# Performance work log

Measured on AMD Instinct MI355X. Metric: run time of the kernel, lower is better.

The kernel has to match this reference:

```python
import jax, jax.numpy as jnp
import numpy as np
import math

D = 512; H = 8; NL = 6; VOCAB = 256; NC = 10; L = 1024; B = 4
DK = D // H
SCALE = math.sqrt(DK)
EMB_SCALE = math.sqrt(D)
EPS = 1e-5


def _pos_encoding(seq_len, d_model):
    pos = jnp.arange(seq_len, dtype=jnp.float32)[:, None]
    div = jnp.exp(-jnp.arange(0, d_model, 2, dtype=jnp.float32) / d_model * math.log(10000.0))
    pe = jnp.zeros((seq_len, d_model), dtype=jnp.float32)
    pe = pe.at[:, 0::2].set(jnp.sin(pos * div))
    pe = pe.at[:, 1::2].set(jnp.cos(pos * div))
    return pe


def _layer_norm(x, g, b):
    m = jnp.mean(x, axis=-1, keepdims=True)
    v = jnp.mean(jnp.square(x - m), axis=-1, keepdims=True)
    return (x - m) * jax.lax.rsqrt(v + EPS) * g + b


def setup_inputs() -> dict:
    key = jax.random.key(0)
    ks = jax.random.split(key, 18)
    s = 0.02  # keep activations in a sane range so softmax is not saturated
    return {
        "tokens": jax.random.randint(ks[0], (B, L), 0, VOCAB, dtype=jnp.int32),
        "emb_table": jax.random.normal(ks[1], (VOCAB, D), jnp.float32) * s,
        "Wq": jax.random.normal(ks[2], (NL, D, D), jnp.float32) * s,
        "bq": jax.random.normal(ks[3], (NL, D), jnp.float32) * s,
        "Wkv": jax.random.normal(ks[4], (NL, 2 * D, D), jnp.float32) * s,
        "bkv": jax.random.normal(ks[5], (NL, 2 * D), jnp.float32) * s,
        "Wo": jax.random.normal(ks[6], (NL, D, D), jnp.float32) * s,
        "bo": jax.random.normal(ks[7], (NL, D), jnp.float32) * s,
        "ln1_g": jnp.ones((NL, D), jnp.float32),
        "ln1_b": jnp.zeros((NL, D), jnp.float32),
        "W1": jax.random.normal(ks[8], (NL, 4 * D, D), jnp.float32) * s,
        "b1": jax.random.normal(ks[9], (NL, 4 * D), jnp.float32) * s,
        "W2": jax.random.normal(ks[10], (NL, D, 4 * D), jnp.float32) * s,
        "b2": jax.random.normal(ks[11], (NL, D), jnp.float32) * s,
        "ln2_g": jnp.ones((NL, D), jnp.float32),
        "ln2_b": jnp.zeros((NL, D), jnp.float32),
        "Wc": jax.random.normal(ks[12], (NC, D), jnp.float32) * s,
        "bc": jax.random.normal(ks[13], (NC,), jnp.float32) * s,
    }


def reference(tokens, emb_table, Wq, bq, Wkv, bkv, Wo, bo, ln1_g, ln1_b,
              W1, b1, W2, b2, ln2_g, ln2_b, Wc, bc):
    seq_len = tokens.shape[1]
    pe = _pos_encoding(seq_len, D)  # [L, D]
    x = emb_table[tokens] * EMB_SCALE + pe[None]  # [B, L, D]  (dropout = identity in eval)

    def block(x, p):
        wq, bq_, wkv, bkv_, wo, bo_, g1, be1, w1, bb1, w2, bb2, g2, be2 = p
        h = _layer_norm(x, g1, be1)
        q = h @ wq.T + bq_                       # [B, L, D]
        kv = h @ wkv.T + bkv_                    # [B, L, 2D]
        k, v = kv[..., :D], kv[..., D:]
        # split heads: [B, H, L, dk]
        q = q.reshape(*q.shape[:2], H, DK).transpose(0, 2, 1, 3)
        k = k.reshape(*k.shape[:2], H, DK).transpose(0, 2, 1, 3)
        v = v.reshape(*v.shape[:2], H, DK).transpose(0, 2, 1, 3)
        score = jnp.einsum('bhqd,bhkd->bhqk', q, k) / SCALE  # [B, H, L, L]
        attn = jax.nn.softmax(score, axis=-1)
        av = jnp.einsum('bhqk,bhkd->bhqd', attn, v)
        av = av.transpose(0, 2, 1, 3).reshape(*x.shape)      # merge heads
        x = x + (av @ wo.T + bo_)
        h2 = _layer_norm(x, g2, be2)
        ffn = jax.nn.relu(h2 @ w1.T + bb1) @ w2.T + bb2
        x = x + ffn
        return x, None

    params = (Wq, bq, Wkv, bkv, Wo, bo, ln1_g, ln1_b, W1, b1, W2, b2, ln2_g, ln2_b)
    x, _ = jax.lax.scan(block, x, params)
    return x @ Wc.T + bc  # [B, L, NC]
```

## Files before the change

### kernel.cpp

```cpp
#include <hip/hip_runtime.h>
#include <math.h>

#define D 512
#define HEADS 8
#define NLAYER 6
#define LSEQ 1024
#define BATCH 4
#define DKH 64
#define MTOK (BATCH*LSEQ)
#define EPS 1e-5f
#define EMB_SCALE 22.627416997969522f
#define INV_SCALE 0.125f

typedef __attribute__((ext_vector_type(8))) __bf16 bf16x8;
typedef __attribute__((ext_vector_type(4))) float f32x4;

__device__ __forceinline__ unsigned short f2bf(float x) {
    union { float f; unsigned u; } v; v.f = x;
    unsigned r = (v.u + 0x7FFFu + ((v.u >> 16) & 1u)) >> 16;
    return (unsigned short)r;
}
__device__ __forceinline__ unsigned pack2(float a, float b) {
    return (unsigned)f2bf(a) | ((unsigned)f2bf(b) << 16);
}
__device__ __forceinline__ void gl_lds16(const unsigned short* g, unsigned short* l) {
    __builtin_amdgcn_global_load_lds(
        (const __attribute__((address_space(1))) unsigned*)g,
        (__attribute__((address_space(3))) unsigned*)l, 16, 0, 0);
}
__device__ __forceinline__ void gload16(bf16x8& d, const unsigned short* p) {
    asm volatile("global_load_dwordx4 %0, %1, off" : "=v"(d) : "v"(p));
}

__global__ __launch_bounds__(128) void embed_kernel(
    const int* __restrict__ tokens, const float* __restrict__ emb,
    float* __restrict__ x)
{
    int row = blockIdx.x;
    int pos = row & (LSEQ - 1);
    int tok = tokens[row];
    int c = threadIdx.x * 4;
    float4 e = *(const float4*)(emb + (size_t)tok * D + c);
    float o[4] = {e.x, e.y, e.z, e.w};
#pragma unroll
    for (int i = 0; i < 4; ++i) {
        int col = c + i;
        int ii = col & ~1;
        float dv = expf(-(float)ii * (9.210340371976184f / (float)D));
        float a = (float)pos * dv;
        float pe = (col & 1) ? cosf(a) : sinf(a);
        o[i] = o[i] * EMB_SCALE + pe;
    }
    float4 r; r.x = o[0]; r.y = o[1]; r.z = o[2]; r.w = o[3];
    *(float4*)(x + (size_t)row * D + c) = r;
}

__global__ __launch_bounds__(256) void ln_kernel(
    const float* __restrict__ x, const float* __restrict__ g,
    const float* __restrict__ b, unsigned short* __restrict__ h)
{
    int lane = threadIdx.x & 63;
    int row = blockIdx.x * 4 + (threadIdx.x >> 6);
    const float* xr = x + (size_t)row * D + lane * 8;
    float4 v0 = *(const float4*)(xr);
    float4 v1 = *(const float4*)(xr + 4);
    float s = v0.x + v0.y + v0.z + v0.w + v1.x + v1.y + v1.z + v1.w;
#pragma unroll
    for (int off = 32; off; off >>= 1) s += __shfl_xor(s, off, 64);
    float m = s * (1.0f / D);
    float d0 = v0.x - m, d1 = v0.y - m, d2 = v0.z - m, d3 = v0.w - m;
    float d4 = v1.x - m, d5 = v1.y - m, d6 = v1.z - m, d7 = v1.w - m;
    float ss = d0*d0 + d1*d1 + d2*d2 + d3*d3 + d4*d4 + d5*d5 + d6*d6 + d7*d7;
#pragma unroll
    for (int off = 32; off; off >>= 1) ss += __shfl_xor(ss, off, 64);
    float inv = rsqrtf(ss * (1.0f / D) + EPS);
    const float* gp = g + lane * 8;
    const float* bp = b + lane * 8;
    float4 g0 = *(const float4*)(gp), g1 = *(const float4*)(gp + 4);
    float4 b0 = *(const float4*)(bp), b1 = *(const float4*)(bp + 4);
    uint4 o;
    o.x = pack2(d0 * inv * g0.x + b0.x, d1 * inv * g0.y + b0.y);
    o.y = pack2(d2 * inv * g0.z + b0.z, d3 * inv * g0.w + b0.w);
    o.z = pack2(d4 * inv * g1.x + b1.x, d5 * inv * g1.y + b1.y);
    o.w = pack2(d6 * inv * g1.z + b1.z, d7 * inv * g1.w + b1.w);
    *(uint4*)(h + (size_t)row * D + lane * 8) = o;
}

__global__ __launch_bounds__(256) void wconv_kernel(
    const float* __restrict__ Wq, const float* __restrict__ Wkv,
    const float* __restrict__ Wo, const float* __restrict__ W1,
    const float* __restrict__ W2, const float* __restrict__ bq,
    const float* __restrict__ bkv, unsigned short* __restrict__ dst,
    float* __restrict__ bias_out)
{
    if (blockIdx.x == 1536) {
        for (int i = threadIdx.x; i < 1536; i += 256)
            bias_out[i] = (i < 512) ? bq[i] : bkv[i - 512];
        return;
    }
    int gid = blockIdx.x * 256 + threadIdx.x;
    int e = gid * 8;
    const float* src;
    if      (e < 262144)  src = Wq  + e;
    else if (e < 786432)  src = Wkv + (e - 262144);
    else if (e < 1048576) src = Wo  + (e - 786432);
    else if (e < 2097152) src = W1  + (e - 1048576);
    else                  src = W2  + (e - 2097152);
    float4 a = *(const float4*)src;
    float4 b = *(const float4*)(src + 4);
    uint4 o;
    o.x = pack2(a.x, a.y); o.y = pack2(a.z, a.w);
    o.z = pack2(b.x, b.y); o.w = pack2(b.z, b.w);
    *(uint4*)(dst + e) = o;
}

template<int OMODE, int BM>
__global__ __launch_bounds__(256) void gemm_bf16(
    const unsigned short* __restrict__ A, const unsigned short* __restrict__ W,
    const float* __restrict__ bias, const float* __restrict__ X,
    void* __restrict__ C, void* __restrict__ C2, void* __restrict__ C3,
    int M, int N, int K)
{
    constexpr int WM = BM / 64;
    constexpr int WN = 4 / WM;
    constexpr int NI = 8 / WN;
    __shared__ __align__(16) unsigned short As[2][BM * 64];
    __shared__ __align__(16) unsigned short Bs[2][128 * 64];
    const int tid = threadIdx.x;
    const int wave = tid >> 6, lane = tid & 63;
    const int quad = lane >> 4, l16 = lane & 15;
    const int wm = wave / WN, wn = wave % WN;
    const int bm = blockIdx.y * BM, bn = blockIdx.x * 128;

    const int rS  = tid >> 3;
    const int csw = (((tid & 7) ^ (rS & 7)) << 3);
    const unsigned short* Asrc = A + (size_t)(bm + rS) * K + csw;
    const unsigned short* Bsrc = W + (size_t)(bn + rS) * K + csw;

    f32x4 acc[4][NI];
#pragma unroll
    for (int mi = 0; mi < 4; ++mi)
#pragma unroll
        for (int ni = 0; ni < NI; ++ni) acc[mi][ni] = (f32x4){0.f, 0.f, 0.f, 0.f};

    const int nt = K >> 6;

#pragma unroll
    for (int i = 0; i < BM / 32; ++i)
        gl_lds16(Asrc + (size_t)(i * 32) * K, &As[0][i * 2048 + tid * 8]);
#pragma unroll
    for (int i = 0; i < 4; ++i)
        gl_lds16(Bsrc + (size_t)(i * 32) * K, &Bs[0][i * 2048 + tid * 8]);
    __syncthreads();

    for (int t = 0; t < nt; ++t) {
        const int cur = t & 1;
        if (t + 1 < nt) {
            const int k0 = (t + 1) << 6;
#pragma unroll
            for (int i = 0; i < BM / 32; ++i)
                gl_lds16(Asrc + (size_t)(i * 32) * K + k0, &As[cur ^ 1][i * 2048 + tid * 8]);
#pragma unroll
            for (int i = 0; i < 4; ++i)
                gl_lds16(Bsrc + (size_t)(i * 32) * K + k0, &Bs[cur ^ 1][i * 2048 + tid * 8]);
        }
#pragma unroll
        for (int kc = 0; kc < 2; ++kc) {
            const int gch = (kc << 2) | quad;
            bf16x8 af[4], bfr[NI];
#pragma unroll
            for (int mi = 0; mi < 4; ++mi) {
                const int ra = wm * 64 + mi * 16 + l16;
                af[mi] = *(const bf16x8*)&As[cur][ra * 64 + ((gch ^ (ra & 7)) << 3)];
            }
#pragma unroll
            for (int ni = 0; ni < NI; ++ni) {
                const int rb = wn * (128 / WN) + ni * 16 + l16;
                bfr[ni] = *(const bf16x8*)&Bs[cur][rb * 64 + ((gch ^ (rb & 7)) << 3)];
            }
#pragma unroll
            for (int mi = 0; mi < 4; ++mi)
#pragma unroll
                for (int ni = 0; ni < NI; ++ni)
                    acc[mi][ni] = __builtin_amdgcn_mfma_f32_16x16x32_bf16(
                        af[mi], bfr[ni], acc[mi][ni], 0, 0, 0);
        }
        __syncthreads();
    }

    const int er = bm + wm * 64;
    const int ec = bn + wn * (128 / WN);

    if (OMODE == 0) {
        float* Cf = (float*)C;
#pragma unroll
        for (int ni = 0; ni < NI; ++ni) {
            int c = ec + ni * 16 + l16;
            float bv = bias[c];
#pragma unroll
            for (int mi = 0; mi < 4; ++mi)
#pragma unroll
                for (int r = 0; r < 4; ++r) {
                    int m = er + mi * 16 + quad * 4 + r;
                    Cf[(size_t)m * N + c] = acc[mi][ni][r] + bv + X[(size_t)m * N + c];
                }
        }
    } else if (OMODE == 1) {
        unsigned short* Cb = (unsigned short*)C;
#pragma unroll
        for (int ni = 0; ni < NI; ++ni) {
            int c = ec + ni * 16 + l16;
            float bv = bias[c];
#pragma unroll
            for (int mi = 0; mi < 4; ++mi)
#pragma unroll
                for (int r = 0; r < 4; ++r) {
                    int m = er + mi * 16 + quad * 4 + r;
                    Cb[(size_t)m * N + c] = f2bf(fmaxf(acc[mi][ni][r] + bv, 0.f));
                }
        }
    } else {
        if (bn < 512) {
            unsigned short* Qp = (unsigned short*)C;
#pragma unroll
            for (int ni = 0; ni < NI; ++ni) {
                int c = ec + ni * 16 + l16;
                float bv = bias[c];
                int hh = c >> 6, dd = c & 63;
                size_t cbase = (size_t)(dd >> 5) * 512 + (size_t)((dd >> 3) & 3) * 128 + (dd & 7);
#pragma unroll
                for (int mi = 0; mi < 4; ++mi)
#pragma unroll
                    for (int r = 0; r < 4; ++r) {
                        int m = er + mi * 16 + quad * 4 + r;
                        int b = m >> 10, t = m & 1023;
                        Qp[(size_t)(b * 8 + hh) * 65536 + (size_t)(t >> 4) * 1024
                           + cbase + (size_t)(t & 15) * 8] =
                            f2bf((acc[mi][ni][r] + bv) * INV_SCALE);
                    }
            }
        } else if (bn < 1024) {
            unsigned short* Kp = (unsigned short*)C2;
#pragma unroll
            for (int ni = 0; ni < NI; ++ni) {
                int c = ec + ni * 16 + l16;
                float bv = bias[c];
                int c2 = c - 512;
                int hh = c2 >> 6, dd = c2 & 63;
                size_t cbase = (size_t)(dd >> 5) * 512 + (size_t)((dd >> 3) & 3) * 128 + (dd & 7);
#pragma unroll
                for (int mi = 0; mi < 4; ++mi)
#pragma unroll
                    for (int r = 0; r < 4; ++r) {
                        int m = er + mi * 16 + quad * 4 + r;
                        int b = m >> 10, t = m & 1023;
                        Kp[(size_t)(b * 8 + hh) * 65536 + (size_t)(t >> 4) * 1024
                           + cbase + (size_t)(t & 15) * 8] =
                            f2bf(acc[mi][ni][r] + bv);
                    }
            }
        } else {
            unsigned short* Vp = (unsigned short*)C3;
#pragma unroll
            for (int ni = 0; ni < NI; ++ni) {
                int c = ec + ni * 16 + l16;
                float bv = bias[c];
                int c2 = c - 1024;
                int hh = c2 >> 6, dd = c2 & 63;
                size_t dbase = (size_t)(dd >> 4) * 16384 + (size_t)(dd & 15) * 8;
#pragma unroll
                for (int mi = 0; mi < 4; ++mi) {
                    int t0 = er + mi * 16 + quad * 4;
                    int b = t0 >> 10, tt = t0 & 1023;
                    ushort4 o;
                    o.x = f2bf(acc[mi][ni][0] + bv);
                    o.y = f2bf(acc[mi][ni][1] + bv);
                    o.z = f2bf(acc[mi][ni][2] + bv);
                    o.w = f2bf(acc[mi][ni][3] + bv);
                    *(ushort4*)(Vp + (size_t)(b * 8 + hh) * 65536 + dbase
                                + (size_t)(tt >> 5) * 512
                                + (size_t)((tt >> 3) & 3) * 128 + (tt & 7)) = o;
                }
            }
        }
    }
}

__global__ __launch_bounds__(256, 1) void attn_mfma(
    const unsigned short* __restrict__ Qb, const unsigned short* __restrict__ Kb,
    const unsigned short* __restrict__ Vt, unsigned short* __restrict__ av)
{
    __shared__ float Ol[4][16][68];
    __shared__ float Ls[4][16];
    const int tid = threadIdx.x;
    const int wave = tid >> 6, lane = tid & 63;
    const int quad = lane >> 4, l16 = lane & 15;
    const int bh = blockIdx.x & 31;
    const int b = bh >> 3, h = bh & 7;
    const int q0 = (blockIdx.x >> 5) * 16;

    const unsigned short* qp = Qb + (size_t)bh * 65536 + (size_t)q0 * 64 + lane * 8;
    const unsigned short* kbase = Kb + (size_t)bh * 65536 + lane * 8;
    const unsigned short* vbase = Vt + (size_t)bh * 65536 + lane * 8;

    const int sA  = ((((2 * quad) & 3) << 4) + l16) << 2;
    const int sB2 = ((((2 * quad + 1) & 3) << 4) + l16) << 2;

    f32x4 o[4];
#pragma unroll
    for (int nf = 0; nf < 4; ++nf) o[nf] = (f32x4){0.f, 0.f, 0.f, 0.f};
    float lp = 0.f;

    const int j0 = wave * 256;

    bf16x8 qf0, qf1;
    gload16(qf0, qp);
    gload16(qf1, qp + 512);

    bf16x8 kc[2][8], vf[2][8];
#pragma unroll
    for (int nf = 0; nf < 4; ++nf) {
        gload16(kc[0][2 * nf],     kbase + (size_t)j0 * 64 + nf * 1024);
        gload16(kc[0][2 * nf + 1], kbase + (size_t)j0 * 64 + nf * 1024 + 512);
        gload16(vf[0][2 * nf],     vbase + (size_t)j0 * 16 + nf * 16384);
        gload16(vf[0][2 * nf + 1], vbase + (size_t)j0 * 16 + nf * 16384 + 512);
    }

#pragma unroll
    for (int it = 0; it < 4; ++it) {
        const int cur = it & 1, nxt = cur ^ 1;
        if (it < 3) {
            const int jn = j0 + (it + 1) * 64;
#pragma unroll
            for (int nf = 0; nf < 4; ++nf) {
                gload16(kc[nxt][2 * nf],     kbase + (size_t)jn * 64 + nf * 1024);
                gload16(kc[nxt][2 * nf + 1], kbase + (size_t)jn * 64 + nf * 1024 + 512);
                gload16(vf[nxt][2 * nf],     vbase + (size_t)jn * 16 + nf * 16384);
                gload16(vf[nxt][2 * nf + 1], vbase + (size_t)jn * 16 + nf * 16384 + 512);
            }
        }
        if (it < 3) asm volatile("s_waitcnt vmcnt(16)" ::: "memory");
        else        asm volatile("s_waitcnt vmcnt(0)"  ::: "memory");
        __builtin_amdgcn_sched_barrier(0);
        f32x4 s[4];
#pragma unroll
        for (int nf = 0; nf < 4; ++nf) {
            f32x4 z = {0.f, 0.f, 0.f, 0.f};
            z = __builtin_amdgcn_mfma_f32_16x16x32_bf16(kc[cur][2 * nf], qf0, z, 0, 0, 0);
            z = __builtin_amdgcn_mfma_f32_16x16x32_bf16(kc[cur][2 * nf + 1], qf1, z, 0, 0, 0);
            s[nf] = z;
        }
        unsigned pk01[4], pk23[4];
#pragma unroll
        for (int nf = 0; nf < 4; ++nf) {
            float p0 = __expf(s[nf][0]);
            float p1 = __expf(s[nf][1]);
            float p2 = __expf(s[nf][2]);
            float p3 = __expf(s[nf][3]);
            lp += (p0 + p1) + (p2 + p3);
            pk01[nf] = pack2(p0, p1);
            pk23[nf] = pack2(p2, p3);
        }
        union PU { unsigned d[4]; bf16x8 v; } f0, f1;
        {
            unsigned a0, a1;
            a0 = (unsigned)__builtin_amdgcn_ds_bpermute(sA,  (int)pk01[0]);
            a1 = (unsigned)__builtin_amdgcn_ds_bpermute(sA,  (int)pk01[1]);
            f0.d[0] = (quad < 2) ? a0 : a1;
            a0 = (unsigned)__builtin_amdgcn_ds_bpermute(sA,  (int)pk23[0]);
            a1 = (unsigned)__builtin_amdgcn_ds_bpermute(sA,  (int)pk23[1]);
            f0.d[1] = (quad < 2) ? a0 : a1;
            a0 = (unsigned)__builtin_amdgcn_ds_bpermute(sB2, (int)pk01[0]);
            a1 = (unsigned)__builtin_amdgcn_ds_bpermute(sB2, (int)pk01[1]);
            f0.d[2] = (quad < 2) ? a0 : a1;
            a0 = (unsigned)__builtin_amdgcn_ds_bpermute(sB2, (int)pk23[0]);
            a1 = (unsigned)__builtin_amdgcn_ds_bpermute(sB2, (int)pk23[1]);
            f0.d[3] = (quad < 2) ? a0 : a1;
            a0 = (unsigned)__builtin_amdgcn_ds_bpermute(sA,  (int)pk01[2]);
            a1 = (unsigned)__builtin_amdgcn_ds_bpermute(sA,  (int)pk01[3]);
            f1.d[0] = (quad < 2) ? a0 : a1;
            a0 = (unsigned)__builtin_amdgcn_ds_bpermute(sA,  (int)pk23[2]);
            a1 = (unsigned)__builtin_amdgcn_ds_bpermute(sA,  (int)pk23[3]);
            f1.d[1] = (quad < 2) ? a0 : a1;
            a0 = (unsigned)__builtin_amdgcn_ds_bpermute(sB2, (int)pk01[2]);
            a1 = (unsigned)__builtin_amdgcn_ds_bpermute(sB2, (int)pk01[3]);
            f1.d[2] = (quad < 2) ? a0 : a1;
            a0 = (unsigned)__builtin_amdgcn_ds_bpermute(sB2, (int)pk23[2]);
            a1 = (unsigned)__builtin_amdgcn_ds_bpermute(sB2, (int)pk23[3]);
            f1.d[3] = (quad < 2) ? a0 : a1;
        }
#pragma unroll
        for (int nf = 0; nf < 4; ++nf) {
            o[nf] = __builtin_amdgcn_mfma_f32_16x16x32_bf16(f0.v, vf[cur][2 * nf], o[nf], 0, 0, 0);
            o[nf] = __builtin_amdgcn_mfma_f32_16x16x32_bf16(f1.v, vf[cur][2 * nf + 1], o[nf], 0, 0, 0);
        }
    }
#pragma unroll
    for (int nf = 0; nf < 4; ++nf)
#pragma unroll
        for (int r = 0; r < 4; ++r)
            Ol[wave][quad * 4 + r][nf * 16 + l16] = o[nf][r];
    float ts = lp;
    ts += __shfl_xor(ts, 16, 64);
    ts += __shfl_xor(ts, 32, 64);
    if (quad == 0) Ls[wave][l16] = ts;
    __syncthreads();
    float denom[4];
#pragma unroll
    for (int r = 0; r < 4; ++r)
        denom[r] = Ls[0][quad * 4 + r] + Ls[1][quad * 4 + r]
                 + Ls[2][quad * 4 + r] + Ls[3][quad * 4 + r];
#pragma unroll
    for (int r = 0; r < 4; ++r) {
        int qq = quad * 4 + r;
        float v = Ol[0][qq][wave * 16 + l16] + Ol[1][qq][wave * 16 + l16]
                + Ol[2][qq][wave * 16 + l16] + Ol[3][qq][wave * 16 + l16];
        int q = q0 + qq;
        av[((size_t)(b * 1024 + q)) * D + h * 64 + wave * 16 + l16] =
            f2bf(v / denom[r]);
    }
}

__global__ __launch_bounds__(256) void cls_kernel(
    const float* __restrict__ x, const float* __restrict__ Wc,
    const float* __restrict__ bc, float* __restrict__ out)
{
    int lane = threadIdx.x & 63;
    int row = blockIdx.x * 4 + (threadIdx.x >> 6);
    const float* xr = x + (size_t)row * D + lane * 8;
    float4 v0 = *(const float4*)xr;
    float4 v1 = *(const float4*)(xr + 4);
    float acc[10];
#pragma unroll
    for (int c = 0; c < 10; ++c) {
        const float* wr = Wc + c * D + lane * 8;
        float4 w0 = *(const float4*)wr;
        float4 w1 = *(const float4*)(wr + 4);
        acc[c] = v0.x*w0.x + v0.y*w0.y + v0.z*w0.z + v0.w*w0.w
               + v1.x*w1.x + v1.y*w1.y + v1.z*w1.z + v1.w*w1.w;
    }
#pragma unroll
    for (int c = 0; c < 10; ++c)
#pragma unroll
        for (int off = 32; off; off >>= 1) acc[c] += __shfl_xor(acc[c], off, 64);
    if (lane == 0) {
#pragma unroll
        for (int c = 0; c < 10; ++c) out[(size_t)row * 10 + c] = acc[c] + bc[c];
    }
}

extern "C" void kernel_launch(void* const* d_in, const int* in_sizes, int n_in,
                              void* d_out, int out_size, void* d_ws, size_t ws_size,
                              hipStream_t stream)
{
    const int*   tokens = (const int*)  d_in[0];
    const float* emb    = (const float*)d_in[1];
    const float* Wq     = (const float*)d_in[2];
    const float* bq     = (const float*)d_in[3];
    const float* Wkv    = (const float*)d_in[4];
    const float* bkv    = (const float*)d_in[5];
    const float* Wo     = (const float*)d_in[6];
    const float* bo     = (const float*)d_in[7];
    const float* ln1g   = (const float*)d_in[8];
    const float* ln1b   = (const float*)d_in[9];
    const float* W1     = (const float*)d_in[10];
    const float* b1     = (const float*)d_in[11];
    const float* W2     = (const float*)d_in[12];
    const float* b2     = (const float*)d_in[13];
    const float* ln2g   = (const float*)d_in[14];
    const float* ln2b   = (const float*)d_in[15];
    const float* Wc     = (const float*)d_in[16];
    const float* bc     = (const float*)d_in[17];
    float* out = (float*)d_out;

    float* x  = (float*)d_ws;
    unsigned short* hb  = (unsigned short*)(x + (size_t)MTOK * D);
    unsigned short* Qb  = hb  + (size_t)MTOK * D;
    unsigned short* Kb  = Qb  + (size_t)32 * 1024 * 64;
    unsigned short* Vt  = Kb  + (size_t)32 * 1024 * 64;
    unsigned short* avb = Vt  + (size_t)32 * 1024 * 64;
    unsigned short* f1b = Qb;
    unsigned short* wl  = avb + (size_t)32 * 1024 * 64;
    float* wbias = (float*)(wl + (size_t)3145728);

    const size_t oWo = 786432, oW1 = 1048576, oW2 = 2097152;

    embed_kernel<<<MTOK, 128, 0, stream>>>(tokens, emb, x);

    for (int l = 0; l < NLAYER; ++l) {
        wconv_kernel<<<1537, 256, 0, stream>>>(
            Wq  + (size_t)l * 262144,  Wkv + (size_t)l * 524288,
            Wo  + (size_t)l * 262144,  W1  + (size_t)l * 1048576,
            W2  + (size_t)l * 1048576, bq + (size_t)l * 512,
            bkv + (size_t)l * 1024, wl, wbias);
        ln_kernel<<<MTOK / 4, 256, 0, stream>>>(x, ln1g + l * D, ln1b + l * D, hb);
        gemm_bf16<2,128><<<dim3(12, 32), 256, 0, stream>>>(
            hb, wl, wbias, nullptr, Qb, Kb, Vt, MTOK, 1536, 512);
        attn_mfma<<<2048, 256, 0, stream>>>(Qb, Kb, Vt, avb);
        gemm_bf16<0,64><<<dim3(4, 64), 256, 0, stream>>>(
            avb, wl + oWo, bo + l * D, x, x, nullptr, nullptr, MTOK, D, D);
        ln_kernel<<<MTOK / 4, 256, 0, stream>>>(x, ln2g + l * D, ln2b + l * D, hb);
        gemm_bf16<1,128><<<dim3(16, 32), 256, 0, stream>>>(
            hb, wl + oW1, b1 + l * 4 * D, nullptr, f1b, nullptr, nullptr, MTOK, 4 * D, D);
        gemm_bf16<0,64><<<dim3(4, 64), 256, 0, stream>>>(
            f1b, wl + oW2, b2 + l * D, x, x, nullptr, nullptr, MTOK, D, 4 * D);
    }

    cls_kernel<<<MTOK / 4, 256, 0, stream>>>(x, Wc, bc, out);
}
```

Before: 842.2 us.

## Process two 16-query tiles per attention block to reuse K/V register loads

Each attention block now handles 32 queries instead of 16, so every K and V fragment loaded into registers feeds two sets of score and output MFMAs. The grid is halved to 1024 blocks and the LDS reduction buffers are doubled. This cuts global K/V traffic per query in half. The cost is more registers and fewer blocks to fill the GPU, which may lower occupancy.

```diff
diff --git a/kernel.cpp b/kernel.cpp
--- a/kernel.cpp
+++ b/kernel.cpp
@@ -290,32 +290,36 @@
     const unsigned short* __restrict__ Qb, const unsigned short* __restrict__ Kb,
     const unsigned short* __restrict__ Vt, unsigned short* __restrict__ av)
 {
-    __shared__ float Ol[4][16][68];
-    __shared__ float Ls[4][16];
+    __shared__ float Ol[4][32][68];
+    __shared__ float Ls[4][32];
     const int tid = threadIdx.x;
     const int wave = tid >> 6, lane = tid & 63;
     const int quad = lane >> 4, l16 = lane & 15;
     const int bh = blockIdx.x & 31;
     const int b = bh >> 3, h = bh & 7;
-    const int q0 = (blockIdx.x >> 5) * 16;
-
-    const unsigned short* qp = Qb + (size_t)bh * 65536 + (size_t)q0 * 64 + lane * 8;
+    const int q0 = (blockIdx.x >> 5) * 32;
+
+    const unsigned short* qp = Qb + (size_t)bh * 65536 + (size_t)(q0 >> 4) * 1024 + lane * 8;
     const unsigned short* kbase = Kb + (size_t)bh * 65536 + lane * 8;
     const unsigned short* vbase = Vt + (size_t)bh * 65536 + lane * 8;
 
     const int sA  = ((((2 * quad) & 3) << 4) + l16) << 2;
     const int sB2 = ((((2 * quad + 1) & 3) << 4) + l16) << 2;
 
-    f32x4 o[4];
-#pragma unroll
-    for (int nf = 0; nf < 4; ++nf) o[nf] = (f32x4){0.f, 0.f, 0.f, 0.f};
-    float lp = 0.f;
+    f32x4 o[2][4];
+#pragma unroll
+    for (int qs = 0; qs < 2; ++qs)
+#pragma unroll
+        for (int nf = 0; nf < 4; ++nf) o[qs][nf] = (f32x4){0.f, 0.f, 0.f, 0.f};
+    float lp[2] = {0.f, 0.f};
 
     const int j0 = wave * 256;
 
-    bf16x8 qf0, qf1;
-    gload16(qf0, qp);
-    gload16(qf1, qp + 512);
+    bf16x8 qf[2][2];
+    gload16(qf[0][0], qp);
+    gload16(qf[0][1], qp + 512);
+    gload16(qf[1][0], qp + 1024);
+    gload16(qf[1][1], qp + 1536);
 
     bf16x8 kc[2][8], vf[2][8];
 #pragma unroll
@@ -342,83 +346,84 @@
         if (it < 3) asm volatile("s_waitcnt vmcnt(16)" ::: "memory");
         else        asm volatile("s_waitcnt vmcnt(0)"  ::: "memory");
         __builtin_amdgcn_sched_barrier(0);
-        f32x4 s[4];
-#pragma unroll
-        for (int nf = 0; nf < 4; ++nf) {
-            f32x4 z = {0.f, 0.f, 0.f, 0.f};
-            z = __builtin_amdgcn_mfma_f32_16x16x32_bf16(kc[cur][2 * nf], qf0, z, 0, 0, 0);
-            z = __builtin_amdgcn_mfma_f32_16x16x32_bf16(kc[cur][2 * nf + 1], qf1, z, 0, 0, 0);
-            s[nf] = z;
-        }
-        unsigned pk01[4], pk23[4];
-#pragma unroll
-        for (int nf = 0; nf < 4; ++nf) {
-            float p0 = __expf(s[nf][0]);
-            float p1 = __expf(s[nf][1]);
-            float p2 = __expf(s[nf][2]);
-            float p3 = __expf(s[nf][3]);
-            lp += (p0 + p1) + (p2 + p3);
-            pk01[nf] = pack2(p0, p1);
-            pk23[nf] = pack2(p2, p3);
-        }
-        union PU { unsigned d[4]; bf16x8 v; } f0, f1;
-        {
+        unsigned pk01[2][4], pk23[2][4];
+#pragma unroll
+        for (int nf = 0; nf < 4; ++nf)
+#pragma unroll
+            for (int qs = 0; qs < 2; ++qs) {
+                f32x4 z = {0.f, 0.f, 0.f, 0.f};
+                z = __builtin_amdgcn_mfma_f32_16x16x32_bf16(kc[cur][2 * nf], qf[qs][0], z, 0, 0, 0);
+                z = __builtin_amdgcn_mfma_f32_16x16x32_bf16(kc[cur][2 * nf + 1], qf[qs][1], z, 0, 0, 0);
+                float p0 = __expf(z[0]);
+                float p1 = __expf(z[1]);
+                float p2 = __expf(z[2]);
+                float p3 = __expf(z[3]);
+                lp[qs] += (p0 + p1) + (p2 + p3);
+                pk01[qs][nf] = pack2(p0, p1);
+                pk23[qs][nf] = pack2(p2, p3);
+            }
+#pragma unroll
+        for (int qs = 0; qs < 2; ++qs) {
+            union PU { unsigned d[4]; bf16x8 v; } f0, f1;
             unsigned a0, a1;
-            a0 = (unsigned)__builtin_amdgcn_ds_bpermute(sA,  (int)pk01[0]);
-            a1 = (unsigned)__builtin_amdgcn_ds_bpermute(sA,  (int)pk01[1]);
+            a0 = (unsigned)__builtin_amdgcn_ds_bpermute(sA,  (int)pk01[qs][0]);
+            a1 = (unsigned)__builtin_amdgcn_ds_bpermute(sA,  (int)pk01[qs][1]);
             f0.d[0] = (quad < 2) ? a0 : a1;
-            a0 = (unsigned)__builtin_amdgcn_ds_bpermute(sA,  (int)pk23[0]);
-            a1 = (unsigned)__builtin_amdgcn_ds_bpermute(sA,  (int)pk23[1]);
+            a0 = (unsigned)__builtin_amdgcn_ds_bpermute(sA,  (int)pk23[qs][0]);
+            a1 = (unsigned)__builtin_amdgcn_ds_bpermute(sA,  (int)pk23[qs][1]);
             f0.d[1] = (quad < 2) ? a0 : a1;
-            a0 = (unsigned)__builtin_amdgcn_ds_bpermute(sB2, (int)pk01[0]);
-            a1 = (unsigned)__builtin_amdgcn_ds_bpermute(sB2, (int)pk01[1]);
+            a0 = (unsigned)__builtin_amdgcn_ds_bpermute(sB2, (int)pk01[qs][0]);
+            a1 = (unsigned)__builtin_amdgcn_ds_bpermute(sB2, (int)pk01[qs][1]);
             f0.d[2] = (quad < 2) ? a0 : a1;
-            a0 = (unsigned)__builtin_amdgcn_ds_bpermute(sB2, (int)pk23[0]);
-            a1 = (unsigned)__builtin_amdgcn_ds_bpermute(sB2, (int)pk23[1]);
+            a0 = (unsigned)__builtin_amdgcn_ds_bpermute(sB2, (int)pk23[qs][0]);
+            a1 = (unsigned)__builtin_amdgcn_ds_bpermute(sB2, (int)pk23[qs][1]);
             f0.d[3] = (quad < 2) ? a0 : a1;
-            a0 = (unsigned)__builtin_amdgcn_ds_bpermute(sA,  (int)pk01[2]);
-            a1 = (unsigned)__builtin_amdgcn_ds_bpermute(sA,  (int)pk01[3]);
+            a0 = (unsigned)__builtin_amdgcn_ds_bpermute(sA,  (int)pk01[qs][2]);
+            a1 = (unsigned)__builtin_amdgcn_ds_bpermute(sA,  (int)pk01[qs][3]);
             f1.d[0] = (quad < 2) ? a0 : a1;
-            a0 = (unsigned)__builtin_amdgcn_ds_bpermute(sA,  (int)pk23[2]);
-            a1 = (unsigned)__builtin_amdgcn_ds_bpermute(sA,  (int)pk23[3]);
+            a0 = (unsigned)__builtin_amdgcn_ds_bpermute(sA,  (int)pk23[qs][2]);
+            a1 = (unsigned)__builtin_amdgcn_ds_bpermute(sA,  (int)pk23[qs][3]);
             f1.d[1] = (quad < 2) ? a0 : a1;
-            a0 = (unsigned)__builtin_amdgcn_ds_bpermute(sB2, (int)pk01[2]);
-            a1 = (unsigned)__builtin_amdgcn_ds_bpermute(sB2, (int)pk01[3]);
+            a0 = (unsigned)__builtin_amdgcn_ds_bpermute(sB2, (int)pk01[qs][2]);
+            a1 = (unsigned)__builtin_amdgcn_ds_bpermute(sB2, (int)pk01[qs][3]);
             f1.d[2] = (quad < 2) ? a0 : a1;
-            a0 = (unsigned)__builtin_amdgcn_ds_bpermute(sB2, (int)pk23[2]);
-            a1 = (unsigned)__builtin_amdgcn_ds_bpermute(sB2, (int)pk23[3]);
+            a0 = (unsigned)__builtin_amdgcn_ds_bpermute(sB2, (int)pk23[qs][2]);
+            a1 = (unsigned)__builtin_amdgcn_ds_bpermute(sB2, (int)pk23[qs][3]);
             f1.d[3] = (quad < 2) ? a0 : a1;
-        }
-#pragma unroll
-        for (int nf = 0; nf < 4; ++nf) {
-            o[nf] = __builtin_amdgcn_mfma_f32_16x16x32_bf16(f0.v, vf[cur][2 * nf], o[nf], 0, 0, 0);
-            o[nf] = __builtin_amdgcn_mfma_f32_16x16x32_bf16(f1.v, vf[cur][2 * nf + 1], o[nf], 0, 0, 0);
-        }
-    }
-#pragma unroll
-    for (int nf = 0; nf < 4; ++nf)
-#pragma unroll
-        for (int r = 0; r < 4; ++r)
-            Ol[wave][quad * 4 + r][nf * 16 + l16] = o[nf][r];
-    float ts = lp;
-    ts += __shfl_xor(ts, 16, 64);
-    ts += __shfl_xor(ts, 32, 64);
-    if (quad == 0) Ls[wave][l16] = ts;
+#pragma unroll
+            for (int nf = 0; nf < 4; ++nf) {
+                o[qs][nf] = __builtin_amdgcn_mfma_f32_16x16x32_bf16(f0.v, vf[cur][2 * nf], o[qs][nf], 0, 0, 0);
+                o[qs][nf] = __builtin_amdgcn_mfma_f32_16x16x32_bf16(f1.v, vf[cur][2 * nf + 1], o[qs][nf], 0, 0, 0);
+            }
+        }
+    }
+#pragma unroll
+    for (int qs = 0; qs < 2; ++qs)
+#pragma unroll
+        for (int nf = 0; nf < 4; ++nf)
+#pragma unroll
+            for (int r = 0; r < 4; ++r)
+                Ol[wave][qs * 16 + quad * 4 + r][nf * 16 + l16] = o[qs][nf][r];
+#pragma unroll
+    for (int qs = 0; qs < 2; ++qs) {
+        float ts = lp[qs];
+        ts += __shfl_xor(ts, 16, 64);
+        ts += __shfl_xor(ts, 32, 64);
+        if (quad == 0) Ls[wave][qs * 16 + l16] = ts;
+    }
     __syncthreads();
-    float denom[4];
-#pragma unroll
-    for (int r = 0; r < 4; ++r)
-        denom[r] = Ls[0][quad * 4 + r] + Ls[1][quad * 4 + r]
-                 + Ls[2][quad * 4 + r] + Ls[3][quad * 4 + r];
-#pragma unroll
-    for (int r = 0; r < 4; ++r) {
-        int qq = quad * 4 + r;
-        float v = Ol[0][qq][wave * 16 + l16] + Ol[1][qq][wave * 16 + l16]
-                + Ol[2][qq][wave * 16 + l16] + Ol[3][qq][wave * 16 + l16];
-        int q = q0 + qq;
-        av[((size_t)(b * 1024 + q)) * D + h * 64 + wave * 16 + l16] =
-            f2bf(v / denom[r]);
-    }
+#pragma unroll
+    for (int half = 0; half < 2; ++half)
+#pragma unroll
+        for (int r = 0; r < 4; ++r) {
+            int qq = half * 16 + quad * 4 + r;
+            float denom = Ls[0][qq] + Ls[1][qq] + Ls[2][qq] + Ls[3][qq];
+            float v = Ol[0][qq][wave * 16 + l16] + Ol[1][qq][wave * 16 + l16]
+                    + Ol[2][qq][wave * 16 + l16] + Ol[3][qq][wave * 16 + l16];
+            int q = q0 + qq;
+            av[((size_t)(b * 1024 + q)) * D + h * 64 + wave * 16 + l16] =
+                f2bf(v / denom);
+        }
 }
 
 __global__ __launch_bounds__(256) void cls_kernel(
@@ -496,7 +501,7 @@
         ln_kernel<<<MTOK / 4, 256, 0, stream>>>(x, ln1g + l * D, ln1b + l * D, hb);
         gemm_bf16<2,128><<<dim3(12, 32), 256, 0, stream>>>(
             hb, wl, wbias, nullptr, Qb, Kb, Vt, MTOK, 1536, 512);
-        attn_mfma<<<2048, 256, 0, stream>>>(Qb, Kb, Vt, avb);
+        attn_mfma<<<1024, 256, 0, stream>>>(Qb, Kb, Vt, avb);
         gemm_bf16<0,64><<<dim3(4, 64), 256, 0, stream>>>(
             avb, wl + oWo, bo + l * D, x, x, nullptr, nullptr, MTOK, D, D);
         ln_kernel<<<MTOK / 4, 256, 0, stream>>>(x, ln2g + l * D, ln2b + l * D, hb);
```

After: 810.8 us. -3.7%, faster.

## Share K/V tiles across waves via LDS in attention, each wave owning queries

Applied to the files above, without the earlier changes.

Restructures the attention kernel so each block handles 64 queries (16 per wave) and walks the full key sequence. K and V tiles are staged once per block into double-buffered LDS with global_load_lds and shared by all four waves. Previously each wave loaded its own quarter of the keys straight from global memory and the partial outputs were combined through LDS. This cuts global K/V traffic by 4x and removes the cross-wave reduction, at the cost of a barrier every iteration and a 4x smaller grid.

```diff
diff --git a/kernel.cpp b/kernel.cpp
--- a/kernel.cpp
+++ b/kernel.cpp
@@ -27,9 +27,6 @@
     __builtin_amdgcn_global_load_lds(
         (const __attribute__((address_space(1))) unsigned*)g,
         (__attribute__((address_space(3))) unsigned*)l, 16, 0, 0);
-}
-__device__ __forceinline__ void gload16(bf16x8& d, const unsigned short* p) {
-    asm volatile("global_load_dwordx4 %0, %1, off" : "=v"(d) : "v"(p));
 }
 
 __global__ __launch_bounds__(128) void embed_kernel(
@@ -286,77 +283,63 @@
     }
 }
 
-__global__ __launch_bounds__(256, 1) void attn_mfma(
+__global__ __launch_bounds__(256, 2) void attn_mfma(
     const unsigned short* __restrict__ Qb, const unsigned short* __restrict__ Kb,
     const unsigned short* __restrict__ Vt, unsigned short* __restrict__ av)
 {
-    __shared__ float Ol[4][16][68];
-    __shared__ float Ls[4][16];
+    __shared__ __align__(16) unsigned short Ks[2][4096];
+    __shared__ __align__(16) unsigned short Vs[2][4096];
     const int tid = threadIdx.x;
     const int wave = tid >> 6, lane = tid & 63;
     const int quad = lane >> 4, l16 = lane & 15;
     const int bh = blockIdx.x & 31;
     const int b = bh >> 3, h = bh & 7;
-    const int q0 = (blockIdx.x >> 5) * 16;
-
-    const unsigned short* qp = Qb + (size_t)bh * 65536 + (size_t)q0 * 64 + lane * 8;
-    const unsigned short* kbase = Kb + (size_t)bh * 65536 + lane * 8;
-    const unsigned short* vbase = Vt + (size_t)bh * 65536 + lane * 8;
+    const int q0 = (blockIdx.x >> 5) * 64 + wave * 16;
+
+    const unsigned short* qp   = Qb + (size_t)bh * 65536 + (size_t)(q0 >> 4) * 1024 + lane * 8;
+    const unsigned short* ksrc = Kb + (size_t)bh * 65536;
+    const unsigned short* vsrc = Vt + (size_t)bh * 65536;
 
     const int sA  = ((((2 * quad) & 3) << 4) + l16) << 2;
     const int sB2 = ((((2 * quad + 1) & 3) << 4) + l16) << 2;
 
+    bf16x8 qf0 = *(const bf16x8*)qp;
+    bf16x8 qf1 = *(const bf16x8*)(qp + 512);
+
     f32x4 o[4];
 #pragma unroll
     for (int nf = 0; nf < 4; ++nf) o[nf] = (f32x4){0.f, 0.f, 0.f, 0.f};
     float lp = 0.f;
 
-    const int j0 = wave * 256;
-
-    bf16x8 qf0, qf1;
-    gload16(qf0, qp);
-    gload16(qf1, qp + 512);
-
-    bf16x8 kc[2][8], vf[2][8];
-#pragma unroll
-    for (int nf = 0; nf < 4; ++nf) {
-        gload16(kc[0][2 * nf],     kbase + (size_t)j0 * 64 + nf * 1024);
-        gload16(kc[0][2 * nf + 1], kbase + (size_t)j0 * 64 + nf * 1024 + 512);
-        gload16(vf[0][2 * nf],     vbase + (size_t)j0 * 16 + nf * 16384);
-        gload16(vf[0][2 * nf + 1], vbase + (size_t)j0 * 16 + nf * 16384 + 512);
-    }
-
-#pragma unroll
-    for (int it = 0; it < 4; ++it) {
-        const int cur = it & 1, nxt = cur ^ 1;
-        if (it < 3) {
-            const int jn = j0 + (it + 1) * 64;
-#pragma unroll
-            for (int nf = 0; nf < 4; ++nf) {
-                gload16(kc[nxt][2 * nf],     kbase + (size_t)jn * 64 + nf * 1024);
-                gload16(kc[nxt][2 * nf + 1], kbase + (size_t)jn * 64 + nf * 1024 + 512);
-                gload16(vf[nxt][2 * nf],     vbase + (size_t)jn * 16 + nf * 16384);
-                gload16(vf[nxt][2 * nf + 1], vbase + (size_t)jn * 16 + nf * 16384 + 512);
-            }
-        }
-        if (it < 3) asm volatile("s_waitcnt vmcnt(16)" ::: "memory");
-        else        asm volatile("s_waitcnt vmcnt(0)"  ::: "memory");
-        __builtin_amdgcn_sched_barrier(0);
-        f32x4 s[4];
+    auto STAGE = [&](int j, int buf) {
+        gl_lds16(ksrc + (size_t)j * 64 + tid * 8,        &Ks[buf][tid * 8]);
+        gl_lds16(ksrc + (size_t)j * 64 + 2048 + tid * 8, &Ks[buf][2048 + tid * 8]);
+        gl_lds16(vsrc + (size_t)j * 16 + (size_t)(wave >> 1) * 16384
+                      + (wave & 1) * 512 + lane * 8,
+                 &Vs[buf][wave * 512 + lane * 8]);
+        gl_lds16(vsrc + (size_t)j * 16 + (size_t)((wave + 4) >> 1) * 16384
+                      + ((wave + 4) & 1) * 512 + lane * 8,
+                 &Vs[buf][2048 + wave * 512 + lane * 8]);
+    };
+
+    STAGE(0, 0);
+    __syncthreads();
+
+    for (int it = 0; it < 16; ++it) {
+        const int cur = it & 1;
+        if (it + 1 < 16) STAGE((it + 1) * 64, cur ^ 1);
+        unsigned pk01[4], pk23[4];
 #pragma unroll
         for (int nf = 0; nf < 4; ++nf) {
+            bf16x8 kc0 = *(const bf16x8*)&Ks[cur][nf * 1024 + lane * 8];
+            bf16x8 kc1 = *(const bf16x8*)&Ks[cur][nf * 1024 + 512 + lane * 8];
             f32x4 z = {0.f, 0.f, 0.f, 0.f};
-            z = __builtin_amdgcn_mfma_f32_16x16x32_bf16(kc[cur][2 * nf], qf0, z, 0, 0, 0);
-            z = __builtin_amdgcn_mfma_f32_16x16x32_bf16(kc[cur][2 * nf + 1], qf1, z, 0, 0, 0);
-            s[nf] = z;
-        }
-        unsigned pk01[4], pk23[4];
-#pragma unroll
-        for (int nf = 0; nf < 4; ++nf) {
-            float p0 = __expf(s[nf][0]);
-            float p1 = __expf(s[nf][1]);
-            float p2 = __expf(s[nf][2]);
-            float p3 = __expf(s[nf][3]);
+            z = __builtin_amdgcn_mfma_f32_16x16x32_bf16(kc0, qf0, z, 0, 0, 0);
+            z = __builtin_amdgcn_mfma_f32_16x16x32_bf16(kc1, qf1, z, 0, 0, 0);
+            float p0 = __expf(z[0]);
+            float p1 = __expf(z[1]);
+            float p2 = __expf(z[2]);
+            float p3 = __expf(z[3]);
             lp += (p0 + p1) + (p2 + p3);
             pk01[nf] = pack2(p0, p1);
             pk23[nf] = pack2(p2, p3);
@@ -391,33 +374,28 @@
         }
 #pragma unroll
         for (int nf = 0; nf < 4; ++nf) {
-            o[nf] = __builtin_amdgcn_mfma_f32_16x16x32_bf16(f0.v, vf[cur][2 * nf], o[nf], 0, 0, 0);
-            o[nf] = __builtin_amdgcn_mfma_f32_16x16x32_bf16(f1.v, vf[cur][2 * nf + 1], o[nf], 0, 0, 0);
-        }
-    }
-#pragma unroll
-    for (int nf = 0; nf < 4; ++nf)
-#pragma unroll
-        for (int r = 0; r < 4; ++r)
-            Ol[wave][quad * 4 + r][nf * 16 + l16] = o[nf][r];
+            bf16x8 vf0 = *(const bf16x8*)&Vs[cur][nf * 1024 + lane * 8];
+            bf16x8 vf1 = *(const bf16x8*)&Vs[cur][nf * 1024 + 512 + lane * 8];
+            o[nf] = __builtin_amdgcn_mfma_f32_16x16x32_bf16(f0.v, vf0, o[nf], 0, 0, 0);
+            o[nf] = __builtin_amdgcn_mfma_f32_16x16x32_bf16(f1.v, vf1, o[nf], 0, 0, 0);
+        }
+        __syncthreads();
+    }
+
     float ts = lp;
     ts += __shfl_xor(ts, 16, 64);
     ts += __shfl_xor(ts, 32, 64);
-    if (quad == 0) Ls[wave][l16] = ts;
-    __syncthreads();
-    float denom[4];
-#pragma unroll
-    for (int r = 0; r < 4; ++r)
-        denom[r] = Ls[0][quad * 4 + r] + Ls[1][quad * 4 + r]
-                 + Ls[2][quad * 4 + r] + Ls[3][quad * 4 + r];
+    union { float f; int i; } tsb; tsb.f = ts;
 #pragma unroll
     for (int r = 0; r < 4; ++r) {
-        int qq = quad * 4 + r;
-        float v = Ol[0][qq][wave * 16 + l16] + Ol[1][qq][wave * 16 + l16]
-                + Ol[2][qq][wave * 16 + l16] + Ol[3][qq][wave * 16 + l16];
-        int q = q0 + qq;
-        av[((size_t)(b * 1024 + q)) * D + h * 64 + wave * 16 + l16] =
-            f2bf(v / denom[r]);
+        union { int i; float f; } dv;
+        dv.i = __builtin_amdgcn_ds_bpermute((quad * 20 + r) << 2, tsb.i);
+        float inv = 1.0f / dv.f;
+        int q = q0 + quad * 4 + r;
+#pragma unroll
+        for (int nf = 0; nf < 4; ++nf)
+            av[((size_t)(b * 1024 + q)) * D + h * 64 + nf * 16 + l16] =
+                f2bf(o[nf][r] * inv);
     }
 }
 
@@ -496,7 +474,7 @@
         ln_kernel<<<MTOK / 4, 256, 0, stream>>>(x, ln1g + l * D, ln1b + l * D, hb);
         gemm_bf16<2,128><<<dim3(12, 32), 256, 0, stream>>>(
             hb, wl, wbias, nullptr, Qb, Kb, Vt, MTOK, 1536, 512);
-        attn_mfma<<<2048, 256, 0, stream>>>(Qb, Kb, Vt, avb);
+        attn_mfma<<<512, 256, 0, stream>>>(Qb, Kb, Vt, avb);
         gemm_bf16<0,64><<<dim3(4, 64), 256, 0, stream>>>(
             avb, wl + oWo, bo + l * D, x, x, nullptr, nullptr, MTOK, D, D);
         ln_kernel<<<MTOK / 4, 256, 0, stream>>>(x, ln2g + l * D, ln2b + l * D, hb);
```

Measured after the change: 815.5 us. 3.2% less time.
